# Optimization experiments

Measured on AMD Instinct MI355X. Metric: run time of the kernel, lower is better.

Reference implementation:

```python
import jax, jax.numpy as jnp
import numpy as np

N_EMBD = 256
N_INPUTS = 66
N_LEVELS = 8
AND_PER_LEVEL = 4096
NOT_PER_LEVEL = 2048
LEVEL = AND_PER_LEVEL + NOT_PER_LEVEL
N_NODES = N_INPUTS + N_LEVELS * LEVEL  # 49218
N_HIDDEN = 4 * N_EMBD  # 1024
N_HID_LAYERS = 8
LN_EPS = 1e-5


def setup_inputs() -> dict:
    rng = np.random.default_rng(0)
    nodes = np.zeros(N_NODES, dtype=np.int32)
    x_edges = np.zeros(N_NODES, dtype=np.int32)
    y_edges = np.zeros(N_NODES, dtype=np.int32)
    for l in range(N_LEVELS):
        s = N_INPUTS + l * LEVEL
        nodes[s:s + AND_PER_LEVEL] = 1           # AND gates
        nodes[s + AND_PER_LEVEL:s + LEVEL] = 2   # NOT gates
        # predecessors strictly earlier in topological order -> valid DAG
        x_edges[s:s + LEVEL] = rng.integers(0, s, LEVEL)
        y_edges[s:s + LEVEL] = rng.integers(0, s, LEVEL)

    key = jax.random.key(0)
    ks = jax.random.split(key, 5)
    s_in = 1.0 / np.sqrt(2 * N_EMBD)
    s_h = 1.0 / np.sqrt(N_HIDDEN)
    return {
        "nodes": jnp.asarray(nodes),
        "x_edges": jnp.asarray(x_edges),
        "y_edges": jnp.asarray(y_edges),
        "input_embd": jax.random.uniform(ks[0], (N_INPUTS, N_EMBD), jnp.float32, -1.0, 1.0),
        "W_in": jax.random.normal(ks[1], (2 * N_EMBD, N_HIDDEN), jnp.float32) * s_in,
        "b_in": jnp.zeros((N_HIDDEN,), jnp.float32),
        "W_hid": jax.random.normal(ks[2], (N_HID_LAYERS, N_HIDDEN, N_HIDDEN), jnp.float32) * s_h,
        "b_hid": jnp.zeros((N_HID_LAYERS, N_HIDDEN), jnp.float32),
        "W_out": jax.random.normal(ks[3], (N_HIDDEN, N_EMBD), jnp.float32) * s_h,
        "b_out": jnp.zeros((N_EMBD,), jnp.float32),
        "ln_g": jnp.ones((N_EMBD,), jnp.float32),
        "ln_b": jnp.zeros((N_EMBD,), jnp.float32),
    }


def _layernorm(x, g, b):
    mu = jnp.mean(x, axis=-1, keepdims=True)
    var = jnp.var(x, axis=-1, keepdims=True)
    return (x - mu) * jax.lax.rsqrt(var + LN_EPS) * g + b


def _mlp(x, W_in, b_in, W_hid, b_hid, W_out, b_out):
    h = jax.nn.relu(x @ W_in + b_in)
    for i in range(N_HID_LAYERS):
        h = jax.nn.relu(h @ W_hid[i] + b_hid[i])
    return h @ W_out + b_out  # dropout p=0.05 is identity in eval mode


def reference(nodes, x_edges, y_edges, input_embd, W_in, b_in, W_hid, b_hid,
              W_out, b_out, ln_g, ln_b):
    # node_embd: [N_NODES, N_EMBD]; input nodes seeded, rest zero
    node_embd = jnp.zeros((N_NODES, N_EMBD), input_embd.dtype).at[:N_INPUTS].set(input_embd)
    # topological wavefronts == contiguous levels in this DAG layout; the torch
    # while-loop processes exactly these sets (order over levels is forced by
    # the x_ready/y_ready dependency tracking), so a static level loop is exact.
    for l in range(N_LEVELS):
        s = N_INPUTS + l * LEVEL
        # NOT gates: negate x-predecessor embedding (processed first, as in torch)
        xn = x_edges[s + AND_PER_LEVEL:s + LEVEL]
        node_embd = node_embd.at[s + AND_PER_LEVEL:s + LEVEL].set(-node_embd[xn])
        # AND gates: LayerNorm(MLP(concat(x_pred, y_pred)))
        xa = x_edges[s:s + AND_PER_LEVEL]
        ya = y_edges[s:s + AND_PER_LEVEL]
        h = jnp.concatenate([node_embd[xa], node_embd[ya]], axis=-1)  # [A, 512]
        out = _layernorm(_mlp(h, W_in, b_in, W_hid, b_hid, W_out, b_out), ln_g, ln_b)
        node_embd = node_embd.at[s:s + AND_PER_LEVEL].set(out)
    return node_embd
```

## Files before the change

kernel.cpp:

```cpp
#include <hip/hip_runtime.h>
#include <hip/hip_bf16.h>
#include <stdint.h>

#define N_EMBD    256
#define N_INPUTS  66
#define N_LEVELS  8
#define APL       4096
#define NPL       2048
#define LVL       6144
#define N_HID     1024

typedef __hip_bfloat16 bf16;
typedef __attribute__((ext_vector_type(8))) short short8;
typedef __attribute__((ext_vector_type(4))) float f32x4;

static __device__ __forceinline__ unsigned short f2b(float f) {
  bf16 h = __float2bfloat16(f);
  return *reinterpret_cast<unsigned short*>(&h);
}

__global__ void k_copy_inputs(const float* __restrict__ in, float* __restrict__ out) {
  int r = blockIdx.x, t = threadIdx.x;
  ((float4*)(out + (size_t)r * 256))[t] = ((const float4*)(in + (size_t)r * 256))[t];
}

__global__ void k_transpose(const float* __restrict__ in, bf16* __restrict__ out, int K, int N) {
  __shared__ float t[32][33];
  size_t boff = (size_t)blockIdx.z * K * N;
  in += boff; out += boff;
  int n0 = blockIdx.x * 32, k0 = blockIdx.y * 32;
  int tx = threadIdx.x, ty = threadIdx.y;
  #pragma unroll
  for (int j = 0; j < 32; j += 8)
    t[ty + j][tx] = in[(size_t)(k0 + ty + j) * N + n0 + tx];
  __syncthreads();
  #pragma unroll
  for (int j = 0; j < 32; j += 8)
    out[(size_t)(n0 + ty + j) * K + k0 + tx] = __float2bfloat16(t[tx][ty + j]);
}

__global__ void k_not_gather(const int* __restrict__ xe, const int* __restrict__ ye,
                             float* __restrict__ node, bf16* __restrict__ H0, int s) {
  int b = blockIdx.x, t = threadIdx.x;
  if (b < NPL) {
    int dst = s + APL + b;
    int src = xe[dst];
    float4 v = ((const float4*)(node + (size_t)src * 256))[t];
    float4 o; o.x = -v.x; o.y = -v.y; o.z = -v.z; o.w = -v.w;
    ((float4*)(node + (size_t)dst * 256))[t] = o;
  } else {
    int r = b - NPL;
    int xa = xe[s + r], ya = ye[s + r];
    float4 vx = ((const float4*)(node + (size_t)xa * 256))[t];
    float4 vy = ((const float4*)(node + (size_t)ya * 256))[t];
    ushort4 ox, oy;
    ox.x = f2b(vx.x); ox.y = f2b(vx.y); ox.z = f2b(vx.z); ox.w = f2b(vx.w);
    oy.x = f2b(vy.x); oy.y = f2b(vy.y); oy.z = f2b(vy.z); oy.w = f2b(vy.w);
    bf16* hr = H0 + (size_t)r * 512;
    ((ushort4*)hr)[t] = ox;
    ((ushort4*)(hr + 256))[t] = oy;
  }
}

template<int BM, int BN, bool RELU, bool BF16OUT>
__global__ __launch_bounds__(256, 2)
void k_gemm(const bf16* __restrict__ A, const bf16* __restrict__ Bt,
            const float* __restrict__ bias, void* __restrict__ Cout,
            int M, int N, int K) {
  constexpr int MT = BM / 32;
  constexpr int NT = BN / 32;
  constexpr int AIT = BM / 32;
  constexpr int BIT = BN / 32;
  constexpr int ABYTES = BM * 128;
  constexpr int BBYTES = BN * 128;
  constexpr int BUF = ABYTES + BBYTES;
  constexpr int LOADS = AIT + BIT;
  __shared__ __align__(16) char smem[2 * BUF];

  const int tid  = threadIdx.x;
  const int lane = tid & 63;
  const int w    = tid >> 6;
  const int wm   = w >> 1, wn = w & 1;
  const int m0 = blockIdx.x * BM;
  const int n0 = blockIdx.y * BN;

  const bf16* gA[AIT];
  const bf16* gB[BIT];
  #pragma unroll
  for (int it = 0; it < AIT; ++it) {
    int ci = it * 256 + tid;
    int r = ci >> 3, g = ci & 7, gs = g ^ (r & 7);
    gA[it] = A + (size_t)(m0 + r) * K + gs * 8;
  }
  #pragma unroll
  for (int it = 0; it < BIT; ++it) {
    int ci = it * 256 + tid;
    int r = ci >> 3, g = ci & 7, gs = g ^ (r & 7);
    gB[it] = Bt + (size_t)(n0 + r) * K + gs * 8;
  }

  int aoff[2][MT], boff[2][NT];
  #pragma unroll
  for (int kk = 0; kk < 2; ++kk) {
    #pragma unroll
    for (int mt = 0; mt < MT; ++mt) {
      int row = wm * (BM / 2) + mt * 16 + (lane & 15);
      int g = kk * 4 + (lane >> 4);
      aoff[kk][mt] = row * 128 + ((g ^ (row & 7)) * 16);
    }
    #pragma unroll
    for (int nt = 0; nt < NT; ++nt) {
      int row = wn * (BN / 2) + nt * 16 + (lane & 15);
      int g = kk * 4 + (lane >> 4);
      boff[kk][nt] = ABYTES + row * 128 + ((g ^ (row & 7)) * 16);
    }
  }

  f32x4 acc[MT][NT] = {};

  auto STAGE = [&](auto bufsel) {
    constexpr int BS = decltype(bufsel)::value;
    char* sA = smem + BS * BUF;
    char* sB = sA + ABYTES;
    #pragma unroll
    for (int it = 0; it < AIT; ++it) {
      __builtin_amdgcn_global_load_lds((const __attribute__((address_space(1))) void*)gA[it],
                                       (__attribute__((address_space(3))) void*)(sA + (it * 256 + w * 64) * 16),
                                       16, 0, 0);
      gA[it] += 64;
    }
    #pragma unroll
    for (int it = 0; it < BIT; ++it) {
      __builtin_amdgcn_global_load_lds((const __attribute__((address_space(1))) void*)gB[it],
                                       (__attribute__((address_space(3))) void*)(sB + (it * 256 + w * 64) * 16),
                                       16, 0, 0);
      gB[it] += 64;
    }
  };

  auto COMPUTE = [&](auto bufsel) {
    constexpr int BS = decltype(bufsel)::value;
    char* base = smem + BS * BUF;
    #pragma unroll
    for (int kk = 0; kk < 2; ++kk) {
      short8 af[MT], bfr[NT];
      #pragma unroll
      for (int mt = 0; mt < MT; ++mt)
        af[mt] = *(const short8*)(base + aoff[kk][mt]);
      #pragma unroll
      for (int nt = 0; nt < NT; ++nt)
        bfr[nt] = *(const short8*)(base + boff[kk][nt]);
      #pragma unroll
      for (int mt = 0; mt < MT; ++mt)
        #pragma unroll
        for (int nt = 0; nt < NT; ++nt)
          acc[mt][nt] = __builtin_amdgcn_mfma_f32_16x16x32_bf16(af[mt], bfr[nt], acc[mt][nt], 0, 0, 0);
    }
  };

  auto WAITC = [&](auto n) {
    constexpr int NW = decltype(n)::value;
    if constexpr (NW == 6)      asm volatile("s_waitcnt vmcnt(6)" ::: "memory");
    else if constexpr (NW == 4) asm volatile("s_waitcnt vmcnt(4)" ::: "memory");
    else                        asm volatile("s_waitcnt vmcnt(0)" ::: "memory");
  };
  constexpr auto C0 = std::integral_constant<int, 0>{};
  constexpr auto C1 = std::integral_constant<int, 1>{};
  constexpr auto CL = std::integral_constant<int, LOADS>{};

  const int nK = K >> 6;
  STAGE(C0);
  STAGE(C1);

  for (int ks2 = 0; ks2 < nK; ks2 += 2) {
    WAITC(CL);
    __builtin_amdgcn_s_barrier();
    COMPUTE(C0);
    __builtin_amdgcn_s_barrier();
    if (ks2 + 2 < nK) STAGE(C0);

    if (ks2 + 2 < nK) WAITC(CL); else WAITC(C0);
    __builtin_amdgcn_s_barrier();
    COMPUTE(C1);
    __builtin_amdgcn_s_barrier();
    if (ks2 + 3 < nK) STAGE(C1);
  }

  #pragma unroll
  for (int nt = 0; nt < NT; ++nt) {
    int col = n0 + wn * (BN / 2) + nt * 16 + (lane & 15);
    float bv = bias[col];
    #pragma unroll
    for (int mt = 0; mt < MT; ++mt) {
      int rbase = m0 + wm * (BM / 2) + mt * 16 + (lane >> 4) * 4;
      #pragma unroll
      for (int r = 0; r < 4; ++r) {
        float v = acc[mt][nt][r] + bv;
        if (RELU) v = fmaxf(v, 0.f);
        if (BF16OUT)
          ((unsigned short*)Cout)[(size_t)(rbase + r) * N + col] = f2b(v);
        else
          ((float*)Cout)[(size_t)(rbase + r) * N + col] = v;
      }
    }
  }
}

__global__ void k_ln(const float* __restrict__ X, const float* __restrict__ g,
                     const float* __restrict__ b, float* __restrict__ node, int s) {
  int r = blockIdx.x;
  int t = threadIdx.x;
  float4 x = ((const float4*)(X + (size_t)r * 256))[t];
  float sm = x.x + x.y + x.z + x.w;
  float sq = x.x * x.x + x.y * x.y + x.z * x.z + x.w * x.w;
  #pragma unroll
  for (int o = 1; o < 64; o <<= 1) { sm += __shfl_xor(sm, o); sq += __shfl_xor(sq, o); }
  float mu  = sm * (1.f / 256.f);
  float var = sq * (1.f / 256.f) - mu * mu;
  float rs  = rsqrtf(var + 1e-5f);
  float4 gv = ((const float4*)g)[t], bv = ((const float4*)b)[t];
  float4 o4;
  o4.x = (x.x - mu) * rs * gv.x + bv.x;
  o4.y = (x.y - mu) * rs * gv.y + bv.y;
  o4.z = (x.z - mu) * rs * gv.z + bv.z;
  o4.w = (x.w - mu) * rs * gv.w + bv.w;
  ((float4*)(node + (size_t)(s + r) * 256))[t] = o4;
}

extern "C" void kernel_launch(void* const* d_in, const int* in_sizes, int n_in,
                              void* d_out, int out_size, void* d_ws, size_t ws_size,
                              hipStream_t stream) {
  const int*   x_edges    = (const int*)d_in[1];
  const int*   y_edges    = (const int*)d_in[2];
  const float* input_embd = (const float*)d_in[3];
  const float* W_in       = (const float*)d_in[4];
  const float* b_in       = (const float*)d_in[5];
  const float* W_hid      = (const float*)d_in[6];
  const float* b_hid      = (const float*)d_in[7];
  const float* W_out      = (const float*)d_in[8];
  const float* b_out      = (const float*)d_in[9];
  const float* ln_g       = (const float*)d_in[10];
  const float* ln_b       = (const float*)d_in[11];
  float* node = (float*)d_out;

  char* ws = (char*)d_ws;
  bf16* WtIn  = (bf16*)(ws);
  bf16* WtHid = (bf16*)(ws + (size_t)1048576);
  bf16* WtOut = (bf16*)(ws + (size_t)17825792);
  bf16* H0    = (bf16*)(ws + (size_t)18350080);
  bf16* HA    = (bf16*)(ws + (size_t)22544384);
  bf16* HB    = (bf16*)(ws + (size_t)30932992);
  float* OutF = (float*)HB;

  k_copy_inputs<<<dim3(66), dim3(64), 0, stream>>>(input_embd, node);

  k_transpose<<<dim3(1024 / 32, 512 / 32, 1), dim3(32, 8), 0, stream>>>(W_in, WtIn, 512, 1024);
  k_transpose<<<dim3(1024 / 32, 1024 / 32, 8), dim3(32, 8), 0, stream>>>(W_hid, WtHid, 1024, 1024);
  k_transpose<<<dim3(256 / 32, 1024 / 32, 1), dim3(32, 8), 0, stream>>>(W_out, WtOut, 1024, 256);

  for (int l = 0; l < N_LEVELS; ++l) {
    int s = N_INPUTS + l * LVL;
    k_not_gather<<<dim3(NPL + APL), dim3(64), 0, stream>>>(x_edges, y_edges, node, H0, s);

    k_gemm<128, 64, true, true><<<dim3(32, 16), dim3(256), 0, stream>>>(H0, WtIn, b_in, HA, 4096, 1024, 512);
    const bf16* src = HA; bf16* dst = HB;
    for (int i = 0; i < 8; ++i) {
      k_gemm<128, 64, true, true><<<dim3(32, 16), dim3(256), 0, stream>>>(
          src, WtHid + (size_t)i * 1024 * 1024, b_hid + i * 1024, dst, 4096, 1024, 1024);
      const bf16* tmp = src; src = dst; dst = (bf16*)tmp;
    }
    k_gemm<64, 64, false, false><<<dim3(64, 4), dim3(256), 0, stream>>>(src, WtOut, b_out, OutF, 4096, 256, 1024);

    k_ln<<<dim3(APL), dim3(64), 0, stream>>>(OutF, ln_g, ln_b, node, s);
  }
}
```

Measured before the change: 961.8 us.

## Load GEMM B operand straight from global into registers, bypassing LDS

The weight (B) operand tiles are no longer staged through shared memory. Each wave now loads its own B fragments directly from global memory into double-buffered registers, prefetching the next K step while the current one computes. Shared memory then holds only the A tiles, and the vmcnt waits are retuned to count only A loads. MFMA issue is also wrapped in s_setprio. This removes LDS traffic and LDS capacity for B, but waves that share columns now fetch duplicate, less coalesced B data from global memory and carry more registers.

```diff
diff --git a/kernel.cpp b/kernel.cpp
--- a/kernel.cpp
+++ b/kernel.cpp
@@ -70,12 +70,8 @@
   constexpr int MT = BM / 32;
   constexpr int NT = BN / 32;
   constexpr int AIT = BM / 32;
-  constexpr int BIT = BN / 32;
   constexpr int ABYTES = BM * 128;
-  constexpr int BBYTES = BN * 128;
-  constexpr int BUF = ABYTES + BBYTES;
-  constexpr int LOADS = AIT + BIT;
-  __shared__ __align__(16) char smem[2 * BUF];
+  __shared__ __align__(16) char smem[2 * ABYTES];
 
   const int tid  = threadIdx.x;
   const int lane = tid & 63;
@@ -85,43 +81,34 @@
   const int n0 = blockIdx.y * BN;
 
   const bf16* gA[AIT];
-  const bf16* gB[BIT];
   #pragma unroll
   for (int it = 0; it < AIT; ++it) {
     int ci = it * 256 + tid;
     int r = ci >> 3, g = ci & 7, gs = g ^ (r & 7);
     gA[it] = A + (size_t)(m0 + r) * K + gs * 8;
   }
-  #pragma unroll
-  for (int it = 0; it < BIT; ++it) {
-    int ci = it * 256 + tid;
-    int r = ci >> 3, g = ci & 7, gs = g ^ (r & 7);
-    gB[it] = Bt + (size_t)(n0 + r) * K + gs * 8;
-  }
-
-  int aoff[2][MT], boff[2][NT];
-  #pragma unroll
-  for (int kk = 0; kk < 2; ++kk) {
+
+  const bf16* pB[NT];
+  #pragma unroll
+  for (int nt = 0; nt < NT; ++nt)
+    pB[nt] = Bt + (size_t)(n0 + wn * (BN / 2) + nt * 16 + (lane & 15)) * K + (lane >> 4) * 8;
+
+  int aoff[2][MT];
+  #pragma unroll
+  for (int kk = 0; kk < 2; ++kk)
     #pragma unroll
     for (int mt = 0; mt < MT; ++mt) {
       int row = wm * (BM / 2) + mt * 16 + (lane & 15);
       int g = kk * 4 + (lane >> 4);
       aoff[kk][mt] = row * 128 + ((g ^ (row & 7)) * 16);
     }
-    #pragma unroll
-    for (int nt = 0; nt < NT; ++nt) {
-      int row = wn * (BN / 2) + nt * 16 + (lane & 15);
-      int g = kk * 4 + (lane >> 4);
-      boff[kk][nt] = ABYTES + row * 128 + ((g ^ (row & 7)) * 16);
-    }
-  }
 
   f32x4 acc[MT][NT] = {};
-
-  auto STAGE = [&](auto bufsel) {
+  short8 bE[NT][2], bO[NT][2];
+
+  auto STAGE_A = [&](auto bufsel) {
     constexpr int BS = decltype(bufsel)::value;
-    char* sA = smem + BS * BUF;
-    char* sB = sA + ABYTES;
+    char* sA = smem + BS * ABYTES;
     #pragma unroll
     for (int it = 0; it < AIT; ++it) {
       __builtin_amdgcn_global_load_lds((const __attribute__((address_space(1))) void*)gA[it],
@@ -129,61 +116,65 @@
                                        16, 0, 0);
       gA[it] += 64;
     }
-    #pragma unroll
-    for (int it = 0; it < BIT; ++it) {
-      __builtin_amdgcn_global_load_lds((const __attribute__((address_space(1))) void*)gB[it],
-                                       (__attribute__((address_space(3))) void*)(sB + (it * 256 + w * 64) * 16),
-                                       16, 0, 0);
-      gB[it] += 64;
-    }
-  };
-
-  auto COMPUTE = [&](auto bufsel) {
+  };
+
+  auto LOADB = [&](short8 (&dst)[NT][2]) {
+    #pragma unroll
+    for (int nt = 0; nt < NT; ++nt) {
+      dst[nt][0] = *(const short8*)(pB[nt]);
+      dst[nt][1] = *(const short8*)(pB[nt] + 32);
+      pB[nt] += 64;
+    }
+  };
+
+  auto COMPUTE = [&](auto bufsel, short8 (&b)[NT][2]) {
     constexpr int BS = decltype(bufsel)::value;
-    char* base = smem + BS * BUF;
+    char* base = smem + BS * ABYTES;
     #pragma unroll
     for (int kk = 0; kk < 2; ++kk) {
-      short8 af[MT], bfr[NT];
+      short8 af[MT];
       #pragma unroll
       for (int mt = 0; mt < MT; ++mt)
         af[mt] = *(const short8*)(base + aoff[kk][mt]);
-      #pragma unroll
-      for (int nt = 0; nt < NT; ++nt)
-        bfr[nt] = *(const short8*)(base + boff[kk][nt]);
+      __builtin_amdgcn_s_setprio(1);
       #pragma unroll
       for (int mt = 0; mt < MT; ++mt)
         #pragma unroll
         for (int nt = 0; nt < NT; ++nt)
-          acc[mt][nt] = __builtin_amdgcn_mfma_f32_16x16x32_bf16(af[mt], bfr[nt], acc[mt][nt], 0, 0, 0);
+          acc[mt][nt] = __builtin_amdgcn_mfma_f32_16x16x32_bf16(af[mt], b[nt][kk], acc[mt][nt], 0, 0, 0);
+      __builtin_amdgcn_s_setprio(0);
     }
   };
 
   auto WAITC = [&](auto n) {
     constexpr int NW = decltype(n)::value;
-    if constexpr (NW == 6)      asm volatile("s_waitcnt vmcnt(6)" ::: "memory");
-    else if constexpr (NW == 4) asm volatile("s_waitcnt vmcnt(4)" ::: "memory");
+    if constexpr (NW == 4)      asm volatile("s_waitcnt vmcnt(4)" ::: "memory");
+    else if constexpr (NW == 2) asm volatile("s_waitcnt vmcnt(2)" ::: "memory");
     else                        asm volatile("s_waitcnt vmcnt(0)" ::: "memory");
   };
   constexpr auto C0 = std::integral_constant<int, 0>{};
   constexpr auto C1 = std::integral_constant<int, 1>{};
-  constexpr auto CL = std::integral_constant<int, LOADS>{};
+  constexpr auto CA = std::integral_constant<int, AIT>{};
 
   const int nK = K >> 6;
-  STAGE(C0);
-  STAGE(C1);
+  STAGE_A(C0);
+  LOADB(bE);
+  STAGE_A(C1);
 
   for (int ks2 = 0; ks2 < nK; ks2 += 2) {
-    WAITC(CL);
-    __builtin_amdgcn_s_barrier();
-    COMPUTE(C0);
-    __builtin_amdgcn_s_barrier();
-    if (ks2 + 2 < nK) STAGE(C0);
-
-    if (ks2 + 2 < nK) WAITC(CL); else WAITC(C0);
-    __builtin_amdgcn_s_barrier();
-    COMPUTE(C1);
-    __builtin_amdgcn_s_barrier();
-    if (ks2 + 3 < nK) STAGE(C1);
+    WAITC(CA);
+    __builtin_amdgcn_s_barrier();
+    LOADB(bO);
+    COMPUTE(C0, bE);
+    __builtin_amdgcn_s_barrier();
+    if (ks2 + 2 < nK) STAGE_A(C0);
+
+    if (ks2 + 2 < nK) WAITC(CA); else WAITC(C0);
+    __builtin_amdgcn_s_barrier();
+    if (ks2 + 2 < nK) LOADB(bE);
+    COMPUTE(C1, bO);
+    __builtin_amdgcn_s_barrier();
+    if (ks2 + 3 < nK) STAGE_A(C1);
   }
 
   #pragma unroll
```

New measurement: 1.738 ms. 1.81x slower.
